# Kernel tuning notes

Measured on AMD Instinct MI355X. Metric: run time of the kernel, lower is better.

The kernel has to match this reference:

```python
import jax, jax.numpy as jnp
import numpy as np

N_NODES = 50000
N_EDGES = 800000
IN_DIM = 256
OUT_DIM = 128
ALPHA = 0.2  # leaky_relu negative slope


def setup_inputs() -> dict:
    key = jax.random.key(0)
    k1, k2, k3, k4, k5 = jax.random.split(key, 5)
    h = jax.random.normal(k1, (N_NODES, IN_DIM), dtype=jnp.float32)
    src = jax.random.randint(k2, (N_EDGES,), 0, N_NODES)
    dst = jax.random.randint(k3, (N_EDGES,), 0, N_NODES)
    W_fc = jax.random.normal(k4, (IN_DIM, OUT_DIM), dtype=jnp.float32) * (1.0 / np.sqrt(IN_DIM))
    attn_w = jax.random.normal(k5, (2 * OUT_DIM,), dtype=jnp.float32) * (1.0 / np.sqrt(2 * OUT_DIM))
    return {"h": h, "src": src, "dst": dst, "W_fc": W_fc, "attn_w": attn_w}


def reference(h, src, dst, W_fc, attn_w):
    n = h.shape[0]
    # fc projection: z = h @ W  -> [N, out]
    z = h @ W_fc
    # edge attention logit: attn_fc(cat(z_src, z_dst)) = z_src@a1 + z_dst@a2
    a1 = attn_w[:OUT_DIM]
    a2 = attn_w[OUT_DIM:]
    logit = z[src] @ a1 + z[dst] @ a2               # [E]
    e = jnp.where(logit >= 0, logit, ALPHA * logit)  # leaky_relu
    # segment softmax over incoming edges of each destination node
    m = jax.ops.segment_max(e, dst, num_segments=n)   # [N], -inf if no edges
    m = jnp.where(jnp.isfinite(m), m, 0.0)
    ex = jnp.exp(e - m[dst])                          # [E]
    denom = jax.ops.segment_sum(ex, dst, num_segments=n)  # [N]
    denom = jnp.where(denom > 0, denom, 1.0)
    alpha_e = ex / denom[dst]                         # [E]
    # weighted scatter-sum of source features
    h_out = jax.ops.segment_sum(alpha_e[:, None] * z[src], dst, num_segments=n)  # [N, out]
    # concat=True -> elu activation
    return jnp.where(h_out > 0, h_out, jnp.expm1(h_out))
```

## Files before the change

### kernel.cpp

```cpp
#include <hip/hip_runtime.h>
#include <math.h>

#define N_NODES 50000
#define N_EDGES 800000
#define IN_DIM 256
#define OUT_DIM 128
#define ALPHA 0.2f

#define BKT 196
#define EPB 4096
#define HIST_NB 196
#define WT_NB   8
#define GEMM_NB 391

typedef __attribute__((ext_vector_type(8))) short short8;
typedef __attribute__((ext_vector_type(4))) float f32x4;

#define OFF_ZB     0u
#define OFF_S1     12800000u
#define OFF_S2     13000000u
#define OFF_OFFS2  13200000u
#define OFF_WT     13400064u
#define OFF_HIST   13465600u
#define OFF_BBT    13619264u
#define OFF_BTOT   13772928u
#define OFF_TMP    13773952u
#define OFF_SRCS   16973952u

static __device__ __forceinline__ unsigned short f2bf_rne(float f) {
    unsigned int u = __float_as_uint(f);
    unsigned int r = (u + 0x7FFFu + ((u >> 16) & 1u)) >> 16;
    return (unsigned short)r;
}
static __device__ __forceinline__ unsigned int pack2bf(float lo, float hi) {
    return (unsigned int)f2bf_rne(lo) | ((unsigned int)f2bf_rne(hi) << 16);
}

__global__ __launch_bounds__(512) void hist_wt(const int* __restrict__ dst,
                                               const float* __restrict__ W,
                                               int* __restrict__ histT,
                                               unsigned short* __restrict__ WT) {
    __shared__ int hcnt[BKT];
    int b = blockIdx.x, t = threadIdx.x;
    if (b < HIST_NB) {
        for (int i = t; i < BKT; i += 512) hcnt[i] = 0;
        __syncthreads();
#pragma unroll
        for (int q = 0; q < 8; q++) {
            int e = b * EPB + q * 512 + t;
            if (e < N_EDGES) atomicAdd(&hcnt[dst[e] >> 8], 1);
        }
        __syncthreads();
        for (int i = t; i < BKT; i += 512) histT[i * HIST_NB + b] = hcnt[i];
    } else {
        int idx = ((b - HIST_NB) * 512 + t) * 8;
        int c = idx >> 8, k0 = idx & 255;
        unsigned int uu[4];
#pragma unroll
        for (int q = 0; q < 4; q++) {
            float lo = W[(size_t)(k0 + 2 * q) * OUT_DIM + c];
            float hi = W[(size_t)(k0 + 2 * q + 1) * OUT_DIM + c];
            uu[q] = pack2bf(lo, hi);
        }
        *(uint4*)(WT + idx) = make_uint4(uu[0], uu[1], uu[2], uu[3]);
    }
}

__global__ __launch_bounds__(256) void colscan(const int* __restrict__ histT,
                                               int* __restrict__ bbaseT,
                                               int* __restrict__ btot) {
    __shared__ int s[256];
    int t = threadIdx.x, b = blockIdx.x;
    int d0 = (t < HIST_NB) ? histT[b * HIST_NB + t] : 0;
    s[t] = d0;
    __syncthreads();
    int v = d0;
    for (int ofs = 1; ofs < 256; ofs <<= 1) {
        int add = (t >= ofs) ? s[t - ofs] : 0;
        __syncthreads();
        v += add;
        s[t] = v;
        __syncthreads();
    }
    if (t < HIST_NB) bbaseT[b * HIST_NB + t] = v - d0;
    if (t == HIST_NB - 1) btot[b] = v;
}

__global__ __launch_bounds__(512) void gemm_scatter(const float* __restrict__ h,
                                                    const unsigned short* __restrict__ WT,
                                                    const float* __restrict__ attn,
                                                    unsigned short* __restrict__ zb,
                                                    float* __restrict__ s1,
                                                    float* __restrict__ s2,
                                                    const int* __restrict__ src,
                                                    const int* __restrict__ dst,
                                                    const int* __restrict__ bbaseT,
                                                    const int* __restrict__ btot,
                                                    unsigned int* __restrict__ tmp) {
    __shared__ char smem[32768];
    const int t = threadIdx.x;

    if (blockIdx.x >= GEMM_NB) {
        int m = blockIdx.x - GEMM_NB;
        int* sS      = (int*)smem;
        int* bbL     = sS + 256;
        int* bstartL = bbL + BKT;
        int* cur     = bstartL + BKT;

        if (t < BKT) { bbL[t] = bbaseT[t * HIST_NB + m]; cur[t] = 0; }
        int d0 = (t < BKT) ? btot[t] : 0;
        if (t < 256) sS[t] = d0;
        __syncthreads();
        int v = d0;
        for (int ofs = 1; ofs < 256; ofs <<= 1) {
            int add = (t < 256 && t >= ofs) ? sS[t - ofs] : 0;
            __syncthreads();
            if (t < 256) { v += add; sS[t] = v; }
            __syncthreads();
        }
        if (t < BKT) bstartL[t] = v - d0;
        __syncthreads();

#pragma unroll
        for (int q = 0; q < 8; q++) {
            int e = m * EPB + q * 512 + t;
            if (e < N_EDGES) {
                int d = dst[e];
                int bkt = d >> 8;
                int r = atomicAdd(&cur[bkt], 1);
                tmp[bstartL[bkt] + bbL[bkt] + r] =
                    ((unsigned int)d << 16) | (unsigned int)src[e];
            }
        }
        return;
    }

    const int lane = t & 63, w = t >> 6;
    const int row0 = blockIdx.x * 128;
    const int m16 = lane & 15, kb = lane >> 4;

    const int rA = row0 + w * 16 + m16;
    const float* hrow = h + (size_t)min(rA, N_NODES - 1) * IN_DIM + kb * 8;

    f32x4 acc[8];
#pragma unroll
    for (int ct = 0; ct < 8; ct++) acc[ct] = (f32x4){0.f, 0.f, 0.f, 0.f};

    float4 v0 = *(const float4*)(hrow);
    float4 v1 = *(const float4*)(hrow + 4);

#pragma unroll
    for (int half = 0; half < 2; half++) {
        if (half) __syncthreads();
#pragma unroll
        for (int q = 0; q < 4; q++) {
            int G = t * 4 + q;
            int cc = G >> 4, gs = G & 15;
            const uint4 v = *(const uint4*)(WT + (size_t)cc * IN_DIM + half * 128 + gs * 8);
            *(uint4*)(smem + cc * 256 + ((gs ^ (cc & 7)) * 16)) = v;
        }
        __syncthreads();
#pragma unroll
        for (int kcl = 0; kcl < 4; kcl++) {
            const float4 c0 = v0, c1 = v1;
            int nk = half * 4 + kcl + 1;
            if (nk < 8) {
                v0 = *(const float4*)(hrow + nk * 32);
                v1 = *(const float4*)(hrow + nk * 32 + 4);
            }
            short8 af;
            af[0] = (short)f2bf_rne(c0.x); af[1] = (short)f2bf_rne(c0.y);
            af[2] = (short)f2bf_rne(c0.z); af[3] = (short)f2bf_rne(c0.w);
            af[4] = (short)f2bf_rne(c1.x); af[5] = (short)f2bf_rne(c1.y);
            af[6] = (short)f2bf_rne(c1.z); af[7] = (short)f2bf_rne(c1.w);
            const char* bbase = smem + m16 * 256 + (((kcl * 4 + kb) ^ (m16 & 7)) * 16);
#pragma unroll
            for (int ct = 0; ct < 8; ct++) {
                const short8 bf = *(const short8*)(bbase + ct * 4096);
                acc[ct] = __builtin_amdgcn_mfma_f32_16x16x32_bf16(af, bf, acc[ct], 0, 0, 0);
            }
        }
    }

    float a1v[8], a2v[8];
#pragma unroll
    for (int ct = 0; ct < 8; ct++) {
        a1v[ct] = attn[ct * 16 + m16];
        a2v[ct] = attn[OUT_DIM + ct * 16 + m16];
    }
#pragma unroll
    for (int i = 0; i < 4; i++) {
        int rr = row0 + w * 16 + kb * 4 + i;
        float q1 = 0.f, q2 = 0.f;
#pragma unroll
        for (int ct = 0; ct < 8; ct++) {
            q1 += acc[ct][i] * a1v[ct];
            q2 += acc[ct][i] * a2v[ct];
        }
        q1 += __shfl_xor(q1, 1); q1 += __shfl_xor(q1, 2);
        q1 += __shfl_xor(q1, 4); q1 += __shfl_xor(q1, 8);
        q2 += __shfl_xor(q2, 1); q2 += __shfl_xor(q2, 2);
        q2 += __shfl_xor(q2, 4); q2 += __shfl_xor(q2, 8);
        if (m16 == 0 && rr < N_NODES) { s1[rr] = q1; s2[rr] = q2; }
        if (rr < N_NODES) {
#pragma unroll
            for (int ct = 0; ct < 8; ct++)
                zb[(size_t)rr * OUT_DIM + ct * 16 + m16] = f2bf_rne(acc[ct][i]);
        }
    }
}

__global__ __launch_bounds__(512) void bucket_sort(const unsigned int* __restrict__ tmp,
                                                   const int* __restrict__ btot,
                                                   unsigned short* __restrict__ srcs,
                                                   int* __restrict__ offs2) {
    __shared__ int sS[256];
    __shared__ int cnt[256];
    __shared__ int cur[256];
    __shared__ int msS, mcS;
    int t = threadIdx.x, b = blockIdx.x;

    int d0 = (t < BKT) ? btot[t] : 0;
    if (t < 256) { sS[t] = d0; cnt[t] = 0; }
    __syncthreads();
    int v = d0;
    for (int ofs = 1; ofs < 256; ofs <<= 1) {
        int add = (t < 256 && t >= ofs) ? sS[t - ofs] : 0;
        __syncthreads();
        if (t < 256) { v += add; sS[t] = v; }
        __syncthreads();
    }
    if (t == b) { msS = v - d0; mcS = d0; }
    __syncthreads();
    const int myStart = msS, myCount = mcS;

    for (int i = t; i < myCount; i += 512)
        atomicAdd(&cnt[(tmp[myStart + i] >> 16) & 255], 1);
    __syncthreads();

    int c0 = 0;
    if (t < 256) { c0 = cnt[t]; sS[t] = c0; }
    __syncthreads();
    int cv = c0;
    for (int ofs = 1; ofs < 256; ofs <<= 1) {
        int add = (t < 256 && t >= ofs) ? sS[t - ofs] : 0;
        __syncthreads();
        if (t < 256) { cv += add; sS[t] = cv; }
        __syncthreads();
    }
    if (t < 256) {
        int excl = cv - c0;
        int node = b * 256 + t;
        if (node < N_NODES) offs2[node] = myStart + excl;
        cur[t] = excl;
    }
    if (b == 0 && t == 0) offs2[N_NODES] = N_EDGES;
    __syncthreads();

    for (int i = t; i < myCount; i += 512) {
        unsigned int u = tmp[myStart + i];
        int r = atomicAdd(&cur[(u >> 16) & 255], 1);
        srcs[myStart + r] = (unsigned short)(u & 0xFFFFu);
    }
}

__global__ __launch_bounds__(256) void aggregate(const unsigned short* __restrict__ zb,
                                                 const int* __restrict__ offs2,
                                                 const unsigned short* __restrict__ srcs,
                                                 const float* __restrict__ s1,
                                                 const float* __restrict__ s2,
                                                 float* __restrict__ out) {
    int wid = (blockIdx.x * blockDim.x + threadIdx.x) >> 6;
    int lane = threadIdx.x & 63;
    if (wid >= N_NODES) return;
    float2* outp = (float2*)(out + (size_t)wid * OUT_DIM) + lane;

    int base = offs2[wid];
    int len = offs2[wid + 1] - base;
    if (len == 0) {
        *outp = make_float2(0.f, 0.f);
        return;
    }
    const float s2v = s2[wid];
    const unsigned int voff = lane * 2;

    float sum = 0.f;
    float ax = 0.f, ay = 0.f;

    for (int c0 = 0; c0 < len; c0 += 64) {
        int i = c0 + lane;
        float ex = 0.f;
        int sj = 0;
        if (i < len) {
            sj = srcs[base + i];
            float lg = s1[sj] + s2v;
            lg = (lg >= 0.f) ? lg : ALPHA * lg;
            ex = __expf(lg);
        }
        sum += ex;
        int cnt = min(64, len - c0);
        int j = 0;
        for (; j + 4 <= cnt; j += 4) {
#pragma unroll
            for (int q = 0; q < 4; q++) {
                int s = __builtin_amdgcn_readlane(sj, j + q);
                float wj = __int_as_float(__builtin_amdgcn_readlane(__float_as_int(ex), j + q));
                unsigned int u = *(const unsigned int*)(zb + (size_t)(unsigned)s * OUT_DIM + voff);
                ax += wj * __uint_as_float(u << 16);
                ay += wj * __uint_as_float(u & 0xFFFF0000u);
            }
        }
        for (; j < cnt; j++) {
            int s = __builtin_amdgcn_readlane(sj, j);
            float wj = __int_as_float(__builtin_amdgcn_readlane(__float_as_int(ex), j));
            unsigned int u = *(const unsigned int*)(zb + (size_t)(unsigned)s * OUT_DIM + voff);
            ax += wj * __uint_as_float(u << 16);
            ay += wj * __uint_as_float(u & 0xFFFF0000u);
        }
    }
#pragma unroll
    for (int m = 32; m >= 1; m >>= 1) sum += __shfl_xor(sum, m);
    float inv = (sum > 0.f) ? 1.f / sum : 1.f;

    float a0 = ax * inv, a1 = ay * inv;
    float2 o;
    o.x = (a0 > 0.f) ? a0 : expm1f(a0);
    o.y = (a1 > 0.f) ? a1 : expm1f(a1);
    *outp = o;
}

extern "C" void kernel_launch(void* const* d_in, const int* in_sizes, int n_in,
                              void* d_out, int out_size, void* d_ws, size_t ws_size,
                              hipStream_t stream) {
    const float* h      = (const float*)d_in[0];
    const int*   src    = (const int*)d_in[1];
    const int*   dst    = (const int*)d_in[2];
    const float* W_fc   = (const float*)d_in[3];
    const float* attn_w = (const float*)d_in[4];
    float* out = (float*)d_out;

    char* ws = (char*)d_ws;
    unsigned short* zb = (unsigned short*)(ws + OFF_ZB);
    float* s1       = (float*)(ws + OFF_S1);
    float* s2       = (float*)(ws + OFF_S2);
    int*   offs2    = (int*)(ws + OFF_OFFS2);
    unsigned short* WT = (unsigned short*)(ws + OFF_WT);
    int*   histT    = (int*)(ws + OFF_HIST);
    int*   bbaseT   = (int*)(ws + OFF_BBT);
    int*   btot     = (int*)(ws + OFF_BTOT);
    unsigned int* tmp = (unsigned int*)(ws + OFF_TMP);
    unsigned short* srcs = (unsigned short*)(ws + OFF_SRCS);

    hist_wt<<<HIST_NB + WT_NB, 512, 0, stream>>>(dst, W_fc, histT, WT);
    colscan<<<BKT, 256, 0, stream>>>(histT, bbaseT, btot);
    gemm_scatter<<<GEMM_NB + HIST_NB, 512, 0, stream>>>(h, WT, attn_w, zb, s1, s2,
                                                        src, dst, bbaseT, btot, tmp);
    bucket_sort<<<BKT, 512, 0, stream>>>(tmp, btot, srcs, offs2);
    aggregate<<<(N_NODES * 64) / 256, 256, 0, stream>>>(zb, offs2, srcs, s1, s2, out);
}
```

Before: 76.23 us.

## Stage bucket scatter in LDS to coalesce global writes of packed edges

The scatter blocks now count edges per bucket locally, compute local bin offsets with a prefix scan, place packed edges into an LDS buffer grouped by bucket, and then write them to global memory with consecutive threads writing consecutive entries within each bucket run. This is meant to replace the random per-edge global stores with mostly contiguous ones. It adds an extra scan, LDS atomics and barriers, and holds the edges in registers between passes.

```diff
diff --git a/kernel.cpp b/kernel.cpp
--- a/kernel.cpp
+++ b/kernel.cpp
@@ -102,14 +102,48 @@
 
     if (blockIdx.x >= GEMM_NB) {
         int m = blockIdx.x - GEMM_NB;
-        int* sS      = (int*)smem;
-        int* bbL     = sS + 256;
-        int* bstartL = bbL + BKT;
-        int* cur     = bstartL + BKT;
-
-        if (t < BKT) { bbL[t] = bbaseT[t * HIST_NB + m]; cur[t] = 0; }
+        int* sS       = (int*)smem;
+        int* binStart = sS + 256;
+        int* cur      = binStart + 256;
+        int* bbL      = cur + 256;
+        int* bstartL  = bbL + BKT;
+        unsigned int* buf = (unsigned int*)(bstartL + BKT);
+
+        const int nv = min(EPB, N_EDGES - m * EPB);
+
+        if (t < 256) cur[t] = 0;
+        if (t < BKT) bbL[t] = bbaseT[t * HIST_NB + m];
+        __syncthreads();
+
+        unsigned int u[8];
+        int nq = 0;
+#pragma unroll
+        for (int q = 0; q < 8; q++) {
+            int e = m * EPB + q * 512 + t;
+            if (e < N_EDGES) {
+                u[nq] = ((unsigned int)dst[e] << 16) | (unsigned int)src[e];
+                atomicAdd(&cur[u[nq] >> 24], 1);
+                nq++;
+            }
+        }
+        __syncthreads();
+
+        int c0 = (t < 256) ? cur[t] : 0;
+        if (t < 256) sS[t] = c0;
+        __syncthreads();
+        int cv = c0;
+        for (int ofs = 1; ofs < 256; ofs <<= 1) {
+            int add = (t < 256 && t >= ofs) ? sS[t - ofs] : 0;
+            __syncthreads();
+            if (t < 256) { cv += add; sS[t] = cv; }
+            __syncthreads();
+        }
+        if (t < 256) binStart[t] = cv - c0;
+        __syncthreads();
+
         int d0 = (t < BKT) ? btot[t] : 0;
         if (t < 256) sS[t] = d0;
+        if (t < 256) cur[t] = binStart[t];
         __syncthreads();
         int v = d0;
         for (int ofs = 1; ofs < 256; ofs <<= 1) {
@@ -121,16 +155,16 @@
         if (t < BKT) bstartL[t] = v - d0;
         __syncthreads();
 
-#pragma unroll
-        for (int q = 0; q < 8; q++) {
-            int e = m * EPB + q * 512 + t;
-            if (e < N_EDGES) {
-                int d = dst[e];
-                int bkt = d >> 8;
-                int r = atomicAdd(&cur[bkt], 1);
-                tmp[bstartL[bkt] + bbL[bkt] + r] =
-                    ((unsigned int)d << 16) | (unsigned int)src[e];
-            }
+        for (int q = 0; q < nq; q++) {
+            int p = atomicAdd(&cur[u[q] >> 24], 1);
+            buf[p] = u[q];
+        }
+        __syncthreads();
+
+        for (int j = t; j < nv; j += 512) {
+            unsigned int w = buf[j];
+            int bkt = w >> 24;
+            tmp[bstartL[bkt] + bbL[bkt] + (j - binStart[bkt])] = w;
         }
         return;
     }
```

Measured after the change: 73.34 us. 1.04x faster.
